# Kernel optimization log

Hardware: AMD Instinct MI355X
Metric: run time of the kernel (lower is better)

Reference implementation:

```python
import jax, jax.numpy as jnp
import numpy as np

B, S, D = 4, 4096, 256  # batch, seq_len, input_dims == num_hiddens
NEG = -1e9

def setup_inputs() -> dict:
    key = jax.random.key(0)
    ks = jax.random.split(key, 9)
    sd = 1.0 / np.sqrt(D)
    x = jax.random.normal(ks[0], (B, S, D), dtype=jnp.float32)
    mask = jnp.tril(jnp.ones((S, S), dtype=jnp.int32))[None, :, :]  # [1,S,S] causal
    # Linear params: y = x @ W.T + b (torch convention); store as [in,out] for einsum
    wq = jax.random.uniform(ks[1], (D, D), jnp.float32, -sd, sd)
    bq = jax.random.uniform(ks[2], (D,), jnp.float32, -sd, sd)
    wk = jax.random.uniform(ks[3], (D, D), jnp.float32, -sd, sd)
    bk = jax.random.uniform(ks[4], (D,), jnp.float32, -sd, sd)
    wv = jax.random.uniform(ks[5], (D, D), jnp.float32, -sd, sd)
    bv = jax.random.uniform(ks[6], (D,), jnp.float32, -sd, sd)
    wo = jax.random.uniform(ks[7], (D, D), jnp.float32, -sd, sd)
    bo = jax.random.uniform(ks[8], (D,), jnp.float32, -sd, sd)
    return {"x": x, "mask": mask, "wq": wq, "bq": bq, "wk": wk, "bk": bk,
            "wv": wv, "bv": bv, "wo": wo, "bo": bo}

def reference(x, mask, wq, bq, wk, bk, wv, bv, wo, bo):
    # Single-head scaled dot-product self-attention (dropout = identity / eval mode)
    q = jnp.einsum('bsd,df->bsf', x, wq) + bq
    k = jnp.einsum('bsd,df->bsf', x, wk) + bk
    v = jnp.einsum('bsd,df->bsf', x, wv) + bv
    attn = jnp.einsum('bqf,bkf->bqk', q, k) / jnp.sqrt(jnp.float32(q.shape[-1]))
    attn = jnp.where(mask == 0, NEG, attn)  # masked_fill(mask==0, -1e9)
    attn = jax.nn.softmax(attn, axis=-1)
    score = jnp.einsum('bqk,bkf->bqf', attn, v)
    out = jnp.einsum('bsf,fd->bsd', score, wo) + bo
    return out
```

## Files before the change

kernel.cpp:

```cpp
#include <hip/hip_runtime.h>
#include <stdint.h>
#include <type_traits>

typedef __attribute__((ext_vector_type(8))) short short8;
typedef __attribute__((ext_vector_type(4))) short s16x4;
typedef __attribute__((ext_vector_type(4))) float f32x4;

#define S_LEN 4096
#define D_DIM 256
#define BATCH 4

__device__ __forceinline__ f32x4 mfma16(short8 a, short8 b, f32x4 c) {
    return __builtin_amdgcn_mfma_f32_16x16x32_bf16(a, b, c, 0, 0, 0);
}

__device__ __forceinline__ short f2bf(float x) {
    uint32_t u = __float_as_uint(x);
    uint32_t r = (u + 0x7FFFu + ((u >> 16) & 1u)) >> 16;
    return (short)r;
}
__device__ __forceinline__ float bf2f(short s) {
    uint32_t u = ((uint32_t)(uint16_t)s) << 16;
    return __uint_as_float(u);
}

__device__ __forceinline__ void gload16(const short* g, short* l) {
    __builtin_amdgcn_global_load_lds(
        (const __attribute__((address_space(1))) void*)g,
        (__attribute__((address_space(3))) void*)l, 16, 0, 0);
}

__global__ __launch_bounds__(256) void xbf_conv(
    const float* __restrict__ x, short* __restrict__ xb)
{
    int i = blockIdx.x * 256 + threadIdx.x;
    f32x4 a = *reinterpret_cast<const f32x4*>(x + (size_t)i * 8);
    f32x4 b = *reinterpret_cast<const f32x4*>(x + (size_t)i * 8 + 4);
    short8 r;
#pragma unroll
    for (int k = 0; k < 4; ++k) r[k] = f2bf(a[k]);
#pragma unroll
    for (int k = 0; k < 4; ++k) r[k + 4] = f2bf(b[k]);
    *reinterpret_cast<short8*>(xb + (size_t)i * 8) = r;
}

__global__ __launch_bounds__(256) void transpose_w(
    const float* __restrict__ wq, const float* __restrict__ wk,
    const float* __restrict__ wv, const float* __restrict__ wo,
    short* __restrict__ out)
{
    __shared__ float t[16][17];
    const float* in = blockIdx.z == 0 ? wq : blockIdx.z == 1 ? wk
                    : blockIdx.z == 2 ? wv : wo;
    short* o = out + (size_t)blockIdx.z * 65536;
    const int x0 = blockIdx.x * 16, y0 = blockIdx.y * 16;
    const int tx = threadIdx.x, ty = threadIdx.y;
    t[ty][tx] = in[(y0 + ty) * 256 + x0 + tx];
    __syncthreads();
    o[(size_t)(x0 + ty) * 256 + y0 + tx] = f2bf(t[tx][ty]);
}

__global__ __launch_bounds__(256) void gemm_qkv(
    const short* __restrict__ A, const short* __restrict__ Bt,
    const float* __restrict__ bq, const float* __restrict__ bk,
    const float* __restrict__ bv,
    short* __restrict__ QF, short* __restrict__ KF, short* __restrict__ VF)
{
    __shared__ short As[128 * 64];
    __shared__ short Bs[128 * 64];
    const int tid = threadIdx.x;
    const int lane = tid & 63;
    const int w = tid >> 6;
    const int wr = w >> 1, wc = w & 1;
    const int lo = lane & 15, hi = lane >> 4;
    const size_t m0 = (size_t)blockIdx.y * 128, n0 = (size_t)blockIdx.x * 128;
    const int reg = (int)(n0 >> 8);
    const float* bias = reg == 0 ? bq : (reg == 1 ? bk : bv);

    f32x4 acc[4][4] = {};

    for (int kt = 0; kt < 4; ++kt) {
#pragma unroll
        for (int i = 0; i < 4; ++i) {
            int c = i * 4 + w;
            int s = c * 64 + lane;
            int row = s >> 3, ke = (s & 7) * 8;
            gload16(A  + (m0 + row) * 256 + kt * 64 + ke, As + c * 512);
            gload16(Bt + (n0 + row) * 256 + kt * 64 + ke, Bs + c * 512);
        }
        __syncthreads();
#pragma unroll
        for (int kk = 0; kk < 2; ++kk) {
            short8 af[4], bf[4];
#pragma unroll
            for (int m = 0; m < 4; ++m)
                af[m] = *reinterpret_cast<const short8*>(&As[(wr * 64 + m * 16 + lo) * 64 + kk * 32 + hi * 8]);
#pragma unroll
            for (int n = 0; n < 4; ++n)
                bf[n] = *reinterpret_cast<const short8*>(&Bs[(wc * 64 + n * 16 + lo) * 64 + kk * 32 + hi * 8]);
#pragma unroll
            for (int m = 0; m < 4; ++m)
#pragma unroll
                for (int n = 0; n < 4; ++n)
                    acc[m][n] = mfma16(af[m], bf[n], acc[m][n]);
        }
        __syncthreads();
    }

#pragma unroll
    for (int m = 0; m < 4; ++m) {
#pragma unroll
        for (int n = 0; n < 4; ++n) {
#pragma unroll
            for (int j = 0; j < 4; ++j) {
                size_t row = m0 + wr * 64 + m * 16 + hi * 4 + j;
                int f = (int)((n0 + wc * 64 + n * 16 + lo) & 255);
                float v = acc[m][n][j] + bias[f];
                int b = (int)(row >> 12), R = (int)(row & 4095);
                if (reg == 0) {
                    int jt = R >> 4, lk = R & 15;
                    int kk = f >> 5, q = f & 31, hk = q >> 3, e = q & 7;
                    QF[((((size_t)(b * 256 + jt) * 8 + kk) * 64) + hk * 16 + lk) * 8 + e] = f2bf(v);
                } else if (reg == 1) {
                    int ktile = R >> 6, nn = (R >> 4) & 3, lk = R & 15;
                    int kk = f >> 5, q = f & 31, hk = q >> 3, e = q & 7;
                    KF[(((((size_t)(b * 64 + ktile) * 8 + kk) * 4 + nn) * 64) + hk * 16 + lk) * 8 + e] = f2bf(v);
                } else {
                    int ktile = R >> 6, t6 = R & 63, k2 = t6 >> 5, r5 = t6 & 31;
                    int hk = r5 >> 3, e = r5 & 7;
                    int nf = f >> 4, lk = f & 15;
                    VF[(((((size_t)(b * 64 + ktile) * 2 + k2) * 16 + nf) * 64) + hk * 16 + lk) * 8 + e] = f2bf(v);
                }
            }
        }
    }
}

__global__ __launch_bounds__(256) void gemm_out(
    const short* __restrict__ A, const short* __restrict__ Bt,
    const float* __restrict__ bias, float* __restrict__ C, int ldc)
{
    __shared__ short As[128 * 64];
    __shared__ short Bs[128 * 64];
    const int tid = threadIdx.x;
    const int lane = tid & 63;
    const int w = tid >> 6;
    const int wr = w >> 1, wc = w & 1;
    const int lo = lane & 15, hi = lane >> 4;
    const size_t m0 = (size_t)blockIdx.y * 128, n0 = (size_t)blockIdx.x * 128;

    f32x4 acc[4][4] = {};

    for (int kt = 0; kt < 4; ++kt) {
#pragma unroll
        for (int i = 0; i < 4; ++i) {
            int c = i * 4 + w;
            int s = c * 64 + lane;
            int row = s >> 3, ke = (s & 7) * 8;
            gload16(A  + (m0 + row) * 256 + kt * 64 + ke, As + c * 512);
            gload16(Bt + (n0 + row) * 256 + kt * 64 + ke, Bs + c * 512);
        }
        __syncthreads();
#pragma unroll
        for (int kk = 0; kk < 2; ++kk) {
            short8 af[4], bf[4];
#pragma unroll
            for (int m = 0; m < 4; ++m)
                af[m] = *reinterpret_cast<const short8*>(&As[(wr * 64 + m * 16 + lo) * 64 + kk * 32 + hi * 8]);
#pragma unroll
            for (int n = 0; n < 4; ++n)
                bf[n] = *reinterpret_cast<const short8*>(&Bs[(wc * 64 + n * 16 + lo) * 64 + kk * 32 + hi * 8]);
#pragma unroll
            for (int m = 0; m < 4; ++m)
#pragma unroll
                for (int n = 0; n < 4; ++n)
                    acc[m][n] = mfma16(af[m], bf[n], acc[m][n]);
        }
        __syncthreads();
    }

#pragma unroll
    for (int m = 0; m < 4; ++m)
#pragma unroll
        for (int n = 0; n < 4; ++n)
#pragma unroll
            for (int j = 0; j < 4; ++j) {
                size_t row = m0 + wr * 64 + m * 16 + hi * 4 + j;
                size_t col = n0 + wc * 64 + n * 16 + lo;
                C[row * (size_t)ldc + col] = acc[m][n][j] + bias[col];
            }
}

template <int NSPLIT>
__global__ __launch_bounds__(128) void calc_sfac(float* __restrict__ PML)
{
    const int bid = (int)blockIdx.x;
    const int lr = threadIdx.x;
    const size_t base = (size_t)bid * NSPLIT;

    float mm[NSPLIT], ll[NSPLIT];
    float M = -3.3e38f;
#pragma unroll
    for (int p = 0; p < NSPLIT; ++p) {
        mm[p] = PML[(base + p) * 256 + lr];
        ll[p] = PML[(base + p) * 256 + 128 + lr];
        M = fmaxf(M, mm[p]);
    }
    float L = 0.f, e[NSPLIT];
#pragma unroll
    for (int p = 0; p < NSPLIT; ++p) { e[p] = __expf(mm[p] - M); L += ll[p] * e[p]; }
    const float inv = 1.0f / L;
#pragma unroll
    for (int p = 0; p < NSPLIT; ++p)
        PML[(base + p) * 256 + lr] = e[p] * inv;
}

template <int NSPLIT>
__global__ __launch_bounds__(256) void gemm_out_fused(
    const short* __restrict__ PO, const float* __restrict__ PML,
    const short* __restrict__ Bt, const float* __restrict__ bias,
    float* __restrict__ C)
{
    __shared__ short As[128 * 64];
    __shared__ short Bs[128 * 64];
    const int tid = threadIdx.x;
    const int lane = tid & 63;
    const int w = tid >> 6;
    const int wr = w >> 1, wc = w & 1;
    const int lo = lane & 15, hi = lane >> 4;
    const size_t m0 = (size_t)blockIdx.y * 128, n0 = (size_t)blockIdx.x * 128;

    f32x4 acc[4][4] = {};

    for (int kt = 0; kt < 4; ++kt) {
        short8 va[4];
#pragma unroll
        for (int i = 0; i < 4; ++i) {
            int c = i * 4 + w;
            int s = c * 64 + lane;
            int row = s >> 3, ke = (s & 7) * 8;
            size_t grow = m0 + row;
            int b = (int)(grow >> 12), R = (int)(grow & 4095);
            int jq = R >> 7, lr = R & 127;
            size_t pb0 = (size_t)(b * 32 + jq) * NSPLIT;

            float a8[8] = {};
#pragma unroll
            for (int p = 0; p < NSPLIT; ++p) {
                float sf = PML[(pb0 + p) * 256 + lr];
                short8 v = *reinterpret_cast<const short8*>(
                    &PO[(pb0 + p) * 32768 + (size_t)lr * 256 + kt * 64 + ke]);
#pragma unroll
                for (int ii = 0; ii < 8; ++ii) a8[ii] += bf2f(v[ii]) * sf;
            }
#pragma unroll
            for (int ii = 0; ii < 8; ++ii) va[i][ii] = f2bf(a8[ii]);

            gload16(Bt + (n0 + row) * 256 + kt * 64 + ke, Bs + c * 512);
        }
#pragma unroll
        for (int i = 0; i < 4; ++i) {
            int c = i * 4 + w;
            *reinterpret_cast<short8*>(&As[(c * 64 + lane) * 8]) = va[i];
        }
        __syncthreads();
#pragma unroll
        for (int kk = 0; kk < 2; ++kk) {
            short8 af[4], bf[4];
#pragma unroll
            for (int m = 0; m < 4; ++m)
                af[m] = *reinterpret_cast<const short8*>(&As[(wr * 64 + m * 16 + lo) * 64 + kk * 32 + hi * 8]);
#pragma unroll
            for (int n = 0; n < 4; ++n)
                bf[n] = *reinterpret_cast<const short8*>(&Bs[(wc * 64 + n * 16 + lo) * 64 + kk * 32 + hi * 8]);
#pragma unroll
            for (int m = 0; m < 4; ++m)
#pragma unroll
                for (int n = 0; n < 4; ++n)
                    acc[m][n] = mfma16(af[m], bf[n], acc[m][n]);
        }
        __syncthreads();
    }

#pragma unroll
    for (int m = 0; m < 4; ++m)
#pragma unroll
        for (int n = 0; n < 4; ++n)
#pragma unroll
            for (int j = 0; j < 4; ++j) {
                size_t row = m0 + wr * 64 + m * 16 + hi * 4 + j;
                size_t col = n0 + wc * 64 + n * 16 + lo;
                C[row * (size_t)256 + col] = acc[m][n][j] + bias[col];
            }
}

template <int NSPLIT, bool DIRECT>
__global__ __launch_bounds__(512) void attn_fwd(
    const short* __restrict__ Qf, const short* __restrict__ Kf,
    const short* __restrict__ Vf, short* __restrict__ PO,
    float* __restrict__ PML, short* __restrict__ Sc)
{
    __shared__ short Ks[2][64 * 256];
    __shared__ short Vs[2][64 * 256];
    __shared__ short P[8][16 * 64];

    const int tid = threadIdx.x;
    const int lane = tid & 63;
    const int w = tid >> 6;
    const int lo = lane & 15, hi = lane >> 4;
    const int bx = (int)blockIdx.x;
    const int m = bx / (BATCH * NSPLIT);
    const int r = bx % (BATCH * NSPLIT);
    const int b = r % BATCH;
    const int p = r / BATCH;

    auto stage = [&](int buf, int kt) {
        const short* Kt = Kf + (size_t)(b * 64 + kt) * 16384;
        const short* Vt = Vf + (size_t)(b * 64 + kt) * 16384;
#pragma unroll
        for (int c4 = 0; c4 < 4; ++c4) {
            int c = c4 * 8 + w;
            gload16(Kt + c * 512 + lane * 8, &Ks[buf][c * 512]);
            gload16(Vt + c * 512 + lane * 8, &Vs[buf][c * 512]);
        }
    };

    for (int half = 0; half < 2; ++half) {
        const int j = half == 0 ? (31 - m) : m;
        const int q0 = j * 128;
        const int last = 2 * j + 1;

        short8 qv[8];
#pragma unroll
        for (int kk = 0; kk < 8; ++kk)
            qv[kk] = *reinterpret_cast<const short8*>(
                Qf + (((size_t)(b * 256 + j * 8 + w) * 8 + kk) * 64 + lane) * 8);

        f32x4 o[16] = {};
        float mrow[4] = {-1e30f, -1e30f, -1e30f, -1e30f};
        float lrow[4] = {0.f, 0.f, 0.f, 0.f};

        int cur = 0;
        if (p <= last) stage(0, p);
        __syncthreads();

        for (int kt = p; kt <= last; kt += NSPLIT) {
            if (kt + NSPLIT <= last) stage(cur ^ 1, kt + NSPLIT);

            f32x4 s4[4] = {};
            __builtin_amdgcn_s_setprio(1);
#pragma unroll
            for (int kk = 0; kk < 8; ++kk) {
#pragma unroll
                for (int n = 0; n < 4; ++n) {
                    short8 kf = *reinterpret_cast<const short8*>(&Ks[cur][((kk * 4 + n) * 64 + lane) * 8]);
                    s4[n] = mfma16(qv[kk], kf, s4[n]);
                }
            }
            __builtin_amdgcn_s_setprio(0);

            const bool diag = (kt >= 2 * j);
            float pm[4] = {-1e30f, -1e30f, -1e30f, -1e30f};
#pragma unroll
            for (int n = 0; n < 4; ++n) {
#pragma unroll
                for (int jj = 0; jj < 4; ++jj) {
                    float v = s4[n][jj] * 0.0625f;
                    if (diag) {
                        int rl = q0 + w * 16 + hi * 4 + jj;
                        int cl = kt * 64 + n * 16 + lo;
                        if (cl > rl) v = -1e30f;
                    }
                    s4[n][jj] = v;
                    pm[jj] = fmaxf(pm[jj], v);
                }
            }
#pragma unroll
            for (int off = 1; off < 16; off <<= 1)
#pragma unroll
                for (int jj = 0; jj < 4; ++jj)
                    pm[jj] = fmaxf(pm[jj], __shfl_xor(pm[jj], off));

            float sc[4], lsum[4];
#pragma unroll
            for (int jj = 0; jj < 4; ++jj) {
                float mn = fmaxf(mrow[jj], pm[jj]);
                sc[jj] = __expf(mrow[jj] - mn);
                mrow[jj] = mn;
                lsum[jj] = 0.f;
            }
#pragma unroll
            for (int n = 0; n < 4; ++n)
#pragma unroll
                for (int jj = 0; jj < 4; ++jj) {
                    float pv = __expf(s4[n][jj] - mrow[jj]);
                    s4[n][jj] = pv;
                    lsum[jj] += pv;
                }
#pragma unroll
            for (int off = 1; off < 16; off <<= 1)
#pragma unroll
                for (int jj = 0; jj < 4; ++jj)
                    lsum[jj] += __shfl_xor(lsum[jj], off);
#pragma unroll
            for (int jj = 0; jj < 4; ++jj)
                lrow[jj] = lrow[jj] * sc[jj] + lsum[jj];
#pragma unroll
            for (int nf = 0; nf < 16; ++nf)
#pragma unroll
                for (int jj = 0; jj < 4; ++jj)
                    o[nf][jj] *= sc[jj];

#pragma unroll
            for (int n = 0; n < 4; ++n)
#pragma unroll
                for (int jj = 0; jj < 4; ++jj) {
                    int row16 = hi * 4 + jj;
                    int idx = (row16 * 64 + (n * 16 + lo)) ^ ((row16 & 7) << 3);
                    P[w][idx] = f2bf(s4[n][jj]);
                }

            __builtin_amdgcn_s_setprio(1);
#pragma unroll
            for (int k2 = 0; k2 < 2; ++k2) {
                short8 pa = *reinterpret_cast<const short8*>(
                    &P[w][(lo * 64 + k2 * 32 + hi * 8) ^ ((lo & 7) << 3)]);
#pragma unroll
                for (int nf = 0; nf < 16; ++nf) {
                    short8 vf = *reinterpret_cast<const short8*>(&Vs[cur][((k2 * 16 + nf) * 64 + lane) * 8]);
                    o[nf] = mfma16(pa, vf, o[nf]);
                }
            }
            __builtin_amdgcn_s_setprio(0);
            __syncthreads();
            cur ^= 1;
        }

        if constexpr (DIRECT) {
            short* Sb = Sc + (size_t)b * S_LEN * D_DIM;
#pragma unroll
            for (int nf = 0; nf < 16; ++nf)
#pragma unroll
                for (int jj = 0; jj < 4; ++jj) {
                    size_t row = q0 + w * 16 + hi * 4 + jj;
                    Sb[row * D_DIM + nf * 16 + lo] = f2bf(o[nf][jj] / lrow[jj]);
                }
        } else {
            size_t pb = (size_t)(b * 32 + j) * NSPLIT + p;
            short* POb = PO + pb * (128 * 256);
            float* PMLb = PML + pb * 256;
#pragma unroll
            for (int nf = 0; nf < 16; ++nf)
#pragma unroll
                for (int jj = 0; jj < 4; ++jj)
                    POb[(w * 16 + hi * 4 + jj) * 256 + nf * 16 + lo] = f2bf(o[nf][jj]);
            if (lo == 0)
#pragma unroll
                for (int jj = 0; jj < 4; ++jj) {
                    PMLb[w * 16 + hi * 4 + jj] = mrow[jj];
                    PMLb[128 + w * 16 + hi * 4 + jj] = lrow[jj];
                }
        }
    }
}

extern "C" void kernel_launch(void* const* d_in, const int* in_sizes, int n_in,
                              void* d_out, int out_size, void* d_ws, size_t ws_size,
                              hipStream_t stream)
{
    const float* x  = (const float*)d_in[0];
    const float* wq = (const float*)d_in[2];
    const float* bq = (const float*)d_in[3];
    const float* wk = (const float*)d_in[4];
    const float* bk = (const float*)d_in[5];
    const float* wv = (const float*)d_in[6];
    const float* bv = (const float*)d_in[7];
    const float* wo = (const float*)d_in[8];
    const float* bo = (const float*)d_in[9];
    float* out = (float*)d_out;

    const size_t NTOK = (size_t)BATCH * S_LEN;
    const size_t TD = NTOK * D_DIM;
    short* WT = (short*)d_ws;
    short* QF = WT + 4 * 65536;
    short* KF = QF + TD;
    short* VF = KF + TD;
    short* xb = VF + TD;
    short* POs = xb;
    short* Sw = QF;
    const size_t po_off_b = (size_t)(4 * 65536 + 3 * TD) * 2;
    const size_t part_b = TD * 2 + (size_t)128 * 256 * 4;
    const size_t xb_end_b = po_off_b + TD * 2;

    const int M = (int)NTOK;

    xbf_conv<<<dim3(2048), 256, 0, stream>>>(x, xb);
    transpose_w<<<dim3(16, 16, 4), dim3(16, 16), 0, stream>>>(wq, wk, wv, wo, WT);
    gemm_qkv<<<dim3(6, M / 128), 256, 0, stream>>>(xb, WT, bq, bk, bv, QF, KF, VF);

    if (ws_size >= po_off_b + 4 * part_b && ws_size >= xb_end_b) {
        float* PML = (float*)(POs + 4 * TD);
        attn_fwd<4, false><<<dim3(16 * BATCH * 4), 512, 0, stream>>>(QF, KF, VF, POs, PML, Sw);
        calc_sfac<4><<<dim3(128), 128, 0, stream>>>(PML);
        gemm_out_fused<4><<<dim3(2, M / 128), 256, 0, stream>>>(POs, PML, WT + 3 * 65536, bo, out);
    } else if (ws_size >= po_off_b + 2 * part_b && ws_size >= xb_end_b) {
        float* PML = (float*)(POs + 2 * TD);
        attn_fwd<2, false><<<dim3(16 * BATCH * 2), 512, 0, stream>>>(QF, KF, VF, POs, PML, Sw);
        calc_sfac<2><<<dim3(128), 128, 0, stream>>>(PML);
        gemm_out_fused<2><<<dim3(2, M / 128), 256, 0, stream>>>(POs, PML, WT + 3 * 65536, bo, out);
    } else {
        attn_fwd<1, true><<<dim3(16 * BATCH), 512, 0, stream>>>(QF, KF, VF, nullptr, nullptr, Sw);
        gemm_out<<<dim3(2, M / 128), 256, 0, stream>>>(Sw, WT + 3 * 65536, bo, out, 256);
    }
}
```

Before: 120.2 us.

## Double-buffer GEMM LDS tiles and fold split-softmax rescale into output GEMM

Adds double-buffered shared-memory tiles to the QKV and output projection GEMMs so the next k-tile's global loads are issued before the current tile's MFMAs, and the per-iteration pre-compute barrier is removed. The separate calc_sfac kernel is deleted. Its max/sum rescale factors are now computed once per row inside gemm_out_fused, which removes one kernel launch and a PML round trip. This doubles LDS use per block, which may lower occupancy, and the scale computation is repeated by both column blocks.

After: 123.3 us. 1.03x slower.

```diff
diff --git a/kernel.cpp b/kernel.cpp
--- a/kernel.cpp
+++ b/kernel.cpp
@@ -66,8 +66,8 @@
     const float* __restrict__ bv,
     short* __restrict__ QF, short* __restrict__ KF, short* __restrict__ VF)
 {
-    __shared__ short As[128 * 64];
-    __shared__ short Bs[128 * 64];
+    __shared__ short As[2][128 * 64];
+    __shared__ short Bs[2][128 * 64];
     const int tid = threadIdx.x;
     const int lane = tid & 63;
     const int w = tid >> 6;
@@ -77,27 +77,34 @@
     const int reg = (int)(n0 >> 8);
     const float* bias = reg == 0 ? bq : (reg == 1 ? bk : bv);
 
-    f32x4 acc[4][4] = {};
-
-    for (int kt = 0; kt < 4; ++kt) {
+    auto stage = [&](int buf, int kt) {
 #pragma unroll
         for (int i = 0; i < 4; ++i) {
             int c = i * 4 + w;
             int s = c * 64 + lane;
             int row = s >> 3, ke = (s & 7) * 8;
-            gload16(A  + (m0 + row) * 256 + kt * 64 + ke, As + c * 512);
-            gload16(Bt + (n0 + row) * 256 + kt * 64 + ke, Bs + c * 512);
-        }
-        __syncthreads();
+            gload16(A  + (m0 + row) * 256 + kt * 64 + ke, &As[buf][c * 512]);
+            gload16(Bt + (n0 + row) * 256 + kt * 64 + ke, &Bs[buf][c * 512]);
+        }
+    };
+
+    f32x4 acc[4][4] = {};
+
+    int cur = 0;
+    stage(0, 0);
+    __syncthreads();
+
+    for (int kt = 0; kt < 4; ++kt) {
+        if (kt < 3) stage(cur ^ 1, kt + 1);
 #pragma unroll
         for (int kk = 0; kk < 2; ++kk) {
             short8 af[4], bf[4];
 #pragma unroll
             for (int m = 0; m < 4; ++m)
-                af[m] = *reinterpret_cast<const short8*>(&As[(wr * 64 + m * 16 + lo) * 64 + kk * 32 + hi * 8]);
+                af[m] = *reinterpret_cast<const short8*>(&As[cur][(wr * 64 + m * 16 + lo) * 64 + kk * 32 + hi * 8]);
 #pragma unroll
             for (int n = 0; n < 4; ++n)
-                bf[n] = *reinterpret_cast<const short8*>(&Bs[(wc * 64 + n * 16 + lo) * 64 + kk * 32 + hi * 8]);
+                bf[n] = *reinterpret_cast<const short8*>(&Bs[cur][(wc * 64 + n * 16 + lo) * 64 + kk * 32 + hi * 8]);
 #pragma unroll
             for (int m = 0; m < 4; ++m)
 #pragma unroll
@@ -105,6 +112,7 @@
                     acc[m][n] = mfma16(af[m], bf[n], acc[m][n]);
         }
         __syncthreads();
+        cur ^= 1;
     }
 
 #pragma unroll
@@ -192,37 +200,13 @@
 }
 
 template <int NSPLIT>
-__global__ __launch_bounds__(128) void calc_sfac(float* __restrict__ PML)
-{
-    const int bid = (int)blockIdx.x;
-    const int lr = threadIdx.x;
-    const size_t base = (size_t)bid * NSPLIT;
-
-    float mm[NSPLIT], ll[NSPLIT];
-    float M = -3.3e38f;
-#pragma unroll
-    for (int p = 0; p < NSPLIT; ++p) {
-        mm[p] = PML[(base + p) * 256 + lr];
-        ll[p] = PML[(base + p) * 256 + 128 + lr];
-        M = fmaxf(M, mm[p]);
-    }
-    float L = 0.f, e[NSPLIT];
-#pragma unroll
-    for (int p = 0; p < NSPLIT; ++p) { e[p] = __expf(mm[p] - M); L += ll[p] * e[p]; }
-    const float inv = 1.0f / L;
-#pragma unroll
-    for (int p = 0; p < NSPLIT; ++p)
-        PML[(base + p) * 256 + lr] = e[p] * inv;
-}
-
-template <int NSPLIT>
 __global__ __launch_bounds__(256) void gemm_out_fused(
     const short* __restrict__ PO, const float* __restrict__ PML,
     const short* __restrict__ Bt, const float* __restrict__ bias,
     float* __restrict__ C)
 {
-    __shared__ short As[128 * 64];
-    __shared__ short Bs[128 * 64];
+    __shared__ short As[2][128 * 64];
+    __shared__ short Bs[2][128 * 64];
     const int tid = threadIdx.x;
     const int lane = tid & 63;
     const int w = tid >> 6;
@@ -230,56 +214,106 @@
     const int lo = lane & 15, hi = lane >> 4;
     const size_t m0 = (size_t)blockIdx.y * 128, n0 = (size_t)blockIdx.x * 128;
 
-    f32x4 acc[4][4] = {};
-
-    for (int kt = 0; kt < 4; ++kt) {
-        short8 va[4];
+    int lrs[4];
+    size_t pb0s[4];
+    float sf[4][NSPLIT];
+#pragma unroll
+    for (int i = 0; i < 4; ++i) {
+        int c = i * 4 + w;
+        int s = c * 64 + lane;
+        int row = s >> 3;
+        size_t grow = m0 + row;
+        int b = (int)(grow >> 12), R = (int)(grow & 4095);
+        int jq = R >> 7, lr = R & 127;
+        size_t pb0 = (size_t)(b * 32 + jq) * NSPLIT;
+        lrs[i] = lr;
+        pb0s[i] = pb0;
+        float mm[NSPLIT], ll[NSPLIT];
+        float M = -3.3e38f;
+#pragma unroll
+        for (int p = 0; p < NSPLIT; ++p) {
+            mm[p] = PML[(pb0 + p) * 256 + lr];
+            ll[p] = PML[(pb0 + p) * 256 + 128 + lr];
+            M = fmaxf(M, mm[p]);
+        }
+        float L = 0.f;
+#pragma unroll
+        for (int p = 0; p < NSPLIT; ++p) { sf[i][p] = __expf(mm[p] - M); L += ll[p] * sf[i][p]; }
+        float inv = 1.0f / L;
+#pragma unroll
+        for (int p = 0; p < NSPLIT; ++p) sf[i][p] *= inv;
+    }
+
+    auto loadA = [&](short8* va, int kt) {
+#pragma unroll
+        for (int i = 0; i < 4; ++i) {
+            int c = i * 4 + w;
+            int s = c * 64 + lane;
+            int ke = (s & 7) * 8;
+            int lr = lrs[i];
+            size_t pb0 = pb0s[i];
+            float a8[8] = {};
+#pragma unroll
+            for (int p = 0; p < NSPLIT; ++p) {
+                short8 v = *reinterpret_cast<const short8*>(
+                    &PO[(pb0 + p) * 32768 + (size_t)lr * 256 + kt * 64 + ke]);
+#pragma unroll
+                for (int ii = 0; ii < 8; ++ii) a8[ii] += bf2f(v[ii]) * sf[i][p];
+            }
+#pragma unroll
+            for (int ii = 0; ii < 8; ++ii) va[i][ii] = f2bf(a8[ii]);
+        }
+    };
+    auto writeA = [&](const short8* va, int buf) {
+#pragma unroll
+        for (int i = 0; i < 4; ++i) {
+            int c = i * 4 + w;
+            *reinterpret_cast<short8*>(&As[buf][(c * 64 + lane) * 8]) = va[i];
+        }
+    };
+    auto stageB = [&](int buf, int kt) {
 #pragma unroll
         for (int i = 0; i < 4; ++i) {
             int c = i * 4 + w;
             int s = c * 64 + lane;
             int row = s >> 3, ke = (s & 7) * 8;
-            size_t grow = m0 + row;
-            int b = (int)(grow >> 12), R = (int)(grow & 4095);
-            int jq = R >> 7, lr = R & 127;
-            size_t pb0 = (size_t)(b * 32 + jq) * NSPLIT;
-
-            float a8[8] = {};
-#pragma unroll
-            for (int p = 0; p < NSPLIT; ++p) {
-                float sf = PML[(pb0 + p) * 256 + lr];
-                short8 v = *reinterpret_cast<const short8*>(
-                    &PO[(pb0 + p) * 32768 + (size_t)lr * 256 + kt * 64 + ke]);
-#pragma unroll
-                for (int ii = 0; ii < 8; ++ii) a8[ii] += bf2f(v[ii]) * sf;
-            }
-#pragma unroll
-            for (int ii = 0; ii < 8; ++ii) va[i][ii] = f2bf(a8[ii]);
-
-            gload16(Bt + (n0 + row) * 256 + kt * 64 + ke, Bs + c * 512);
-        }
-#pragma unroll
-        for (int i = 0; i < 4; ++i) {
-            int c = i * 4 + w;
-            *reinterpret_cast<short8*>(&As[(c * 64 + lane) * 8]) = va[i];
-        }
-        __syncthreads();
+            gload16(Bt + (n0 + row) * 256 + kt * 64 + ke, &Bs[buf][c * 512]);
+        }
+    };
+
+    f32x4 acc[4][4] = {};
+
+    short8 va0[4];
+    loadA(va0, 0);
+    stageB(0, 0);
+    writeA(va0, 0);
+    __syncthreads();
+
+    int cur = 0;
+    for (int kt = 0; kt < 4; ++kt) {
+        short8 vn[4];
+        if (kt < 3) {
+            loadA(vn, kt + 1);
+            stageB(cur ^ 1, kt + 1);
+        }
 #pragma unroll
         for (int kk = 0; kk < 2; ++kk) {
             short8 af[4], bf[4];
 #pragma unroll
             for (int m = 0; m < 4; ++m)
-                af[m] = *reinterpret_cast<const short8*>(&As[(wr * 64 + m * 16 + lo) * 64 + kk * 32 + hi * 8]);
+                af[m] = *reinterpret_cast<const short8*>(&As[cur][(wr * 64 + m * 16 + lo) * 64 + kk * 32 + hi * 8]);
 #pragma unroll
             for (int n = 0; n < 4; ++n)
-                bf[n] = *reinterpret_cast<const short8*>(&Bs[(wc * 64 + n * 16 + lo) * 64 + kk * 32 + hi * 8]);
+                bf[n] = *reinterpret_cast<const short8*>(&Bs[cur][(wc * 64 + n * 16 + lo) * 64 + kk * 32 + hi * 8]);
 #pragma unroll
             for (int m = 0; m < 4; ++m)
 #pragma unroll
                 for (int n = 0; n < 4; ++n)
                     acc[m][n] = mfma16(af[m], bf[n], acc[m][n]);
         }
+        if (kt < 3) writeA(vn, cur ^ 1);
         __syncthreads();
+        cur ^= 1;
     }
 
 #pragma unroll
@@ -501,12 +535,10 @@
     if (ws_size >= po_off_b + 4 * part_b && ws_size >= xb_end_b) {
         float* PML = (float*)(POs + 4 * TD);
         attn_fwd<4, false><<<dim3(16 * BATCH * 4), 512, 0, stream>>>(QF, KF, VF, POs, PML, Sw);
-        calc_sfac<4><<<dim3(128), 128, 0, stream>>>(PML);
         gemm_out_fused<4><<<dim3(2, M / 128), 256, 0, stream>>>(POs, PML, WT + 3 * 65536, bo, out);
     } else if (ws_size >= po_off_b + 2 * part_b && ws_size >= xb_end_b) {
         float* PML = (float*)(POs + 2 * TD);
         attn_fwd<2, false><<<dim3(16 * BATCH * 2), 512, 0, stream>>>(QF, KF, VF, POs, PML, Sw);
-        calc_sfac<2><<<dim3(128), 128, 0, stream>>>(PML);
         gemm_out_fused<2><<<dim3(2, M / 128), 256, 0, stream>>>(POs, PML, WT + 3 * 65536, bo, out);
     } else {
         attn_fwd<1, true><<<dim3(16 * BATCH), 512, 0, stream>>>(QF, KF, VF, nullptr, nullptr, Sw);
```

## Add 1024-thread attention kernel with 256-row query tiles and 8-way KV split

Applied to the files above, without the earlier changes.

Adds an attention kernel that uses 16 waves per block to process 256 query rows per tile, paired as tile j and 15-j so causal work is balanced. The key range is split eight ways, and partial results go to a larger workspace. The softmax-rescale and output-GEMM kernels are templated on rows per tile, so they can combine the new partials. The aim is more reuse of each K/V tile across query rows and better load balance. The cost is more partial-output traffic in the combine step, and V is now single-buffered, which adds a sync stall.

Measured after the change: 222.3 us. +85.0%, slower.

```diff
diff --git a/kernel.cpp b/kernel.cpp
--- a/kernel.cpp
+++ b/kernel.cpp
@@ -191,8 +191,8 @@
             }
 }
 
-template <int NSPLIT>
-__global__ __launch_bounds__(128) void calc_sfac(float* __restrict__ PML)
+template <int NSPLIT, int ROWS>
+__global__ void calc_sfac(float* __restrict__ PML)
 {
     const int bid = (int)blockIdx.x;
     const int lr = threadIdx.x;
@@ -202,8 +202,8 @@
     float M = -3.3e38f;
 #pragma unroll
     for (int p = 0; p < NSPLIT; ++p) {
-        mm[p] = PML[(base + p) * 256 + lr];
-        ll[p] = PML[(base + p) * 256 + 128 + lr];
+        mm[p] = PML[(base + p) * (2 * ROWS) + lr];
+        ll[p] = PML[(base + p) * (2 * ROWS) + ROWS + lr];
         M = fmaxf(M, mm[p]);
     }
     float L = 0.f, e[NSPLIT];
@@ -212,10 +212,10 @@
     const float inv = 1.0f / L;
 #pragma unroll
     for (int p = 0; p < NSPLIT; ++p)
-        PML[(base + p) * 256 + lr] = e[p] * inv;
-}
-
-template <int NSPLIT>
+        PML[(base + p) * (2 * ROWS) + lr] = e[p] * inv;
+}
+
+template <int NSPLIT, int ROWS, int JBLK>
 __global__ __launch_bounds__(256) void gemm_out_fused(
     const short* __restrict__ PO, const float* __restrict__ PML,
     const short* __restrict__ Bt, const float* __restrict__ bias,
@@ -241,15 +241,15 @@
             int row = s >> 3, ke = (s & 7) * 8;
             size_t grow = m0 + row;
             int b = (int)(grow >> 12), R = (int)(grow & 4095);
-            int jq = R >> 7, lr = R & 127;
-            size_t pb0 = (size_t)(b * 32 + jq) * NSPLIT;
+            int jq = R / ROWS, lr = R % ROWS;
+            size_t pb0 = (size_t)(b * JBLK + jq) * NSPLIT;
 
             float a8[8] = {};
 #pragma unroll
             for (int p = 0; p < NSPLIT; ++p) {
-                float sf = PML[(pb0 + p) * 256 + lr];
+                float sf = PML[(pb0 + p) * (2 * ROWS) + lr];
                 short8 v = *reinterpret_cast<const short8*>(
-                    &PO[(pb0 + p) * 32768 + (size_t)lr * 256 + kt * 64 + ke]);
+                    &PO[(pb0 + p) * ((size_t)ROWS * 256) + (size_t)lr * 256 + kt * 64 + ke]);
 #pragma unroll
                 for (int ii = 0; ii < 8; ++ii) a8[ii] += bf2f(v[ii]) * sf;
             }
@@ -292,6 +292,174 @@
                 size_t col = n0 + wc * 64 + n * 16 + lo;
                 C[row * (size_t)256 + col] = acc[m][n][j] + bias[col];
             }
+}
+
+template <int NSPLIT>
+__global__ __launch_bounds__(1024) void attn_big(
+    const short* __restrict__ Qf, const short* __restrict__ Kf,
+    const short* __restrict__ Vf, short* __restrict__ PO,
+    float* __restrict__ PML)
+{
+    __shared__ short Ks[2][64 * 256];
+    __shared__ short Vs[64 * 256];
+    __shared__ short P[16][16 * 64];
+
+    const int tid = threadIdx.x;
+    const int lane = tid & 63;
+    const int w = tid >> 6;
+    const int lo = lane & 15, hi = lane >> 4;
+    const int bx = (int)blockIdx.x;
+    const int m = bx / (BATCH * NSPLIT);
+    const int r = bx % (BATCH * NSPLIT);
+    const int b = r % BATCH;
+    const int p = r / BATCH;
+
+    auto stageK = [&](int buf, int kt) {
+        const short* Kt = Kf + (size_t)(b * 64 + kt) * 16384;
+#pragma unroll
+        for (int c4 = 0; c4 < 2; ++c4) {
+            int c = c4 * 16 + w;
+            gload16(Kt + c * 512 + lane * 8, &Ks[buf][c * 512]);
+        }
+    };
+    auto stageV = [&](int kt) {
+        const short* Vt = Vf + (size_t)(b * 64 + kt) * 16384;
+#pragma unroll
+        for (int c4 = 0; c4 < 2; ++c4) {
+            int c = c4 * 16 + w;
+            gload16(Vt + c * 512 + lane * 8, &Vs[c * 512]);
+        }
+    };
+
+    for (int half = 0; half < 2; ++half) {
+        const int j = half == 0 ? (15 - m) : m;
+        const int q0 = j * 256;
+        const int last = 4 * j + 3;
+
+        short8 qv[8];
+#pragma unroll
+        for (int kk = 0; kk < 8; ++kk)
+            qv[kk] = *reinterpret_cast<const short8*>(
+                Qf + (((size_t)(b * 256 + j * 16 + w) * 8 + kk) * 64 + lane) * 8);
+
+        f32x4 o[16] = {};
+        float mrow[4] = {-1e30f, -1e30f, -1e30f, -1e30f};
+        float lrow[4] = {0.f, 0.f, 0.f, 0.f};
+
+        int cur = 0;
+        if (p <= last) stageK(0, p);
+        __syncthreads();
+
+        for (int kt = p; kt <= last; kt += NSPLIT) {
+            stageV(kt);
+            if (kt + NSPLIT <= last) stageK(cur ^ 1, kt + NSPLIT);
+
+            f32x4 s4[4] = {};
+            __builtin_amdgcn_s_setprio(1);
+#pragma unroll
+            for (int kk = 0; kk < 8; ++kk) {
+#pragma unroll
+                for (int n = 0; n < 4; ++n) {
+                    short8 kf = *reinterpret_cast<const short8*>(&Ks[cur][((kk * 4 + n) * 64 + lane) * 8]);
+                    s4[n] = mfma16(qv[kk], kf, s4[n]);
+                }
+            }
+            __builtin_amdgcn_s_setprio(0);
+
+            const bool diag = (kt >= 4 * j);
+            float pm[4] = {-1e30f, -1e30f, -1e30f, -1e30f};
+#pragma unroll
+            for (int n = 0; n < 4; ++n) {
+#pragma unroll
+                for (int jj = 0; jj < 4; ++jj) {
+                    float v = s4[n][jj] * 0.0625f;
+                    if (diag) {
+                        int rl = q0 + w * 16 + hi * 4 + jj;
+                        int cl = kt * 64 + n * 16 + lo;
+                        if (cl > rl) v = -1e30f;
+                    }
+                    s4[n][jj] = v;
+                    pm[jj] = fmaxf(pm[jj], v);
+                }
+            }
+#pragma unroll
+            for (int off = 1; off < 16; off <<= 1)
+#pragma unroll
+                for (int jj = 0; jj < 4; ++jj)
+                    pm[jj] = fmaxf(pm[jj], __shfl_xor(pm[jj], off));
+
+            float sc[4], lsum[4];
+#pragma unroll
+            for (int jj = 0; jj < 4; ++jj) {
+                float mn = fmaxf(mrow[jj], pm[jj]);
+                sc[jj] = __expf(mrow[jj] - mn);
+                mrow[jj] = mn;
+                lsum[jj] = 0.f;
+            }
+#pragma unroll
+            for (int n = 0; n < 4; ++n)
+#pragma unroll
+                for (int jj = 0; jj < 4; ++jj) {
+                    float pv = __expf(s4[n][jj] - mrow[jj]);
+                    s4[n][jj] = pv;
+                    lsum[jj] += pv;
+                }
+#pragma unroll
+            for (int off = 1; off < 16; off <<= 1)
+#pragma unroll
+                for (int jj = 0; jj < 4; ++jj)
+                    lsum[jj] += __shfl_xor(lsum[jj], off);
+#pragma unroll
+            for (int jj = 0; jj < 4; ++jj)
+                lrow[jj] = lrow[jj] * sc[jj] + lsum[jj];
+#pragma unroll
+            for (int nf = 0; nf < 16; ++nf)
+#pragma unroll
+                for (int jj = 0; jj < 4; ++jj)
+                    o[nf][jj] *= sc[jj];
+
+#pragma unroll
+            for (int n = 0; n < 4; ++n)
+#pragma unroll
+                for (int jj = 0; jj < 4; ++jj) {
+                    int row16 = hi * 4 + jj;
+                    int idx = (row16 * 64 + (n * 16 + lo)) ^ ((row16 & 7) << 3);
+                    P[w][idx] = f2bf(s4[n][jj]);
+                }
+
+            __syncthreads();
+
+            __builtin_amdgcn_s_setprio(1);
+#pragma unroll
+            for (int k2 = 0; k2 < 2; ++k2) {
+                short8 pa = *reinterpret_cast<const short8*>(
+                    &P[w][(lo * 64 + k2 * 32 + hi * 8) ^ ((lo & 7) << 3)]);
+#pragma unroll
+                for (int nf = 0; nf < 16; ++nf) {
+                    short8 vf = *reinterpret_cast<const short8*>(&Vs[((k2 * 16 + nf) * 64 + lane) * 8]);
+                    o[nf] = mfma16(pa, vf, o[nf]);
+                }
+            }
+            __builtin_amdgcn_s_setprio(0);
+            __syncthreads();
+            cur ^= 1;
+        }
+
+        size_t pb = (size_t)(b * 16 + j) * NSPLIT + p;
+        short* POb = PO + pb * (256 * 256);
+        float* PMLb = PML + pb * 512;
+#pragma unroll
+        for (int nf = 0; nf < 16; ++nf)
+#pragma unroll
+            for (int jj = 0; jj < 4; ++jj)
+                POb[(w * 16 + hi * 4 + jj) * 256 + nf * 16 + lo] = f2bf(o[nf][jj]);
+        if (lo == 0)
+#pragma unroll
+            for (int jj = 0; jj < 4; ++jj) {
+                PMLb[w * 16 + hi * 4 + jj] = mrow[jj];
+                PMLb[256 + w * 16 + hi * 4 + jj] = lrow[jj];
+            }
+    }
 }
 
 template <int NSPLIT, bool DIRECT>
@@ -489,8 +657,11 @@
     short* POs = xb;
     short* Sw = QF;
     const size_t po_off_b = (size_t)(4 * 65536 + 3 * TD) * 2;
+    const size_t xb_end_b = po_off_b + TD * 2;
+
+    const size_t big_need = po_off_b + (size_t)512 * 131072 + (size_t)512 * 2048;
     const size_t part_b = TD * 2 + (size_t)128 * 256 * 4;
-    const size_t xb_end_b = po_off_b + TD * 2;
+    const size_t r17_need = po_off_b + 4 * part_b;
 
     const int M = (int)NTOK;
 
@@ -498,16 +669,16 @@
     transpose_w<<<dim3(16, 16, 4), dim3(16, 16), 0, stream>>>(wq, wk, wv, wo, WT);
     gemm_qkv<<<dim3(6, M / 128), 256, 0, stream>>>(xb, WT, bq, bk, bv, QF, KF, VF);
 
-    if (ws_size >= po_off_b + 4 * part_b && ws_size >= xb_end_b) {
+    if (ws_size >= big_need && ws_size >= xb_end_b) {
+        float* PML = (float*)(POs + (size_t)512 * 65536);
+        attn_big<8><<<dim3(8 * BATCH * 8), 1024, 0, stream>>>(QF, KF, VF, POs, PML);
+        calc_sfac<8, 256><<<dim3(64), 256, 0, stream>>>(PML);
+        gemm_out_fused<8, 256, 16><<<dim3(2, M / 128), 256, 0, stream>>>(POs, PML, WT + 3 * 65536, bo, out);
+    } else if (ws_size >= r17_need && ws_size >= xb_end_b) {
         float* PML = (float*)(POs + 4 * TD);
         attn_fwd<4, false><<<dim3(16 * BATCH * 4), 512, 0, stream>>>(QF, KF, VF, POs, PML, Sw);
-        calc_sfac<4><<<dim3(128), 128, 0, stream>>>(PML);
-        gemm_out_fused<4><<<dim3(2, M / 128), 256, 0, stream>>>(POs, PML, WT + 3 * 65536, bo, out);
-    } else if (ws_size >= po_off_b + 2 * part_b && ws_size >= xb_end_b) {
-        float* PML = (float*)(POs + 2 * TD);
-        attn_fwd<2, false><<<dim3(16 * BATCH * 2), 512, 0, stream>>>(QF, KF, VF, POs, PML, Sw);
-        calc_sfac<2><<<dim3(128), 128, 0, stream>>>(PML);
-        gemm_out_fused<2><<<dim3(2, M / 128), 256, 0, stream>>>(POs, PML, WT + 3 * 65536, bo, out);
+        calc_sfac<4, 128><<<dim3(128), 128, 0, stream>>>(PML);
+        gemm_out_fused<4, 128, 32><<<dim3(2, M / 128), 256, 0, stream>>>(POs, PML, WT + 3 * 65536, bo, out);
     } else {
         attn_fwd<1, true><<<dim3(16 * BATCH), 512, 0, stream>>>(QF, KF, VF, nullptr, nullptr, Sw);
         gemm_out<<<dim3(2, M / 128), 256, 0, stream>>>(Sw, WT + 3 * 65536, bo, out, 256);
```
